# Optimization experiments

Measured on AMD Instinct MI355X. Metric: run time of the kernel, lower is better.

Reference implementation:

```python
import jax, jax.numpy as jnp
import numpy as np
import math

BT, N, D, H = 16, 1024, 128, 8
HD = D // H


def setup_inputs() -> dict:
    key = jax.random.key(0)
    ks = jax.random.split(key, 12)
    s = 1.0 / math.sqrt(D)
    return {
        "x": jax.random.normal(ks[0], (BT, N, D), dtype=jnp.float32),
        "adj": jax.random.uniform(ks[1], (BT, N, N), dtype=jnp.float32),
        "Wq": jax.random.normal(ks[2], (D, D), dtype=jnp.float32) * s,
        "bq": jax.random.normal(ks[3], (D,), dtype=jnp.float32) * 0.01,
        "Wk": jax.random.normal(ks[4], (D, D), dtype=jnp.float32) * s,
        "bk": jax.random.normal(ks[5], (D,), dtype=jnp.float32) * 0.01,
        "Wv": jax.random.normal(ks[6], (D, D), dtype=jnp.float32) * s,
        "bv": jax.random.normal(ks[7], (D,), dtype=jnp.float32) * 0.01,
        "Wo": jax.random.normal(ks[8], (D, D), dtype=jnp.float32) * s,
        "bo": jax.random.normal(ks[9], (D,), dtype=jnp.float32) * 0.01,
    }


def reference(x, adj, Wq, bq, Wk, bk, Wv, bv, Wo, bo):
    bt, n, d = x.shape
    # projections (torch Linear: x @ W.T + b), split into heads -> (BT,H,N,HD)
    q = (x @ Wq.T + bq).reshape(bt, n, H, HD).transpose(0, 2, 1, 3)
    k = (x @ Wk.T + bk).reshape(bt, n, H, HD).transpose(0, 2, 1, 3)
    v = (x @ Wv.T + bv).reshape(bt, n, H, HD).transpose(0, 2, 1, 3)
    scores = jnp.einsum('bhnd,bhmd->bhnm', q, k) / math.sqrt(HD)  # (BT,H,N,N)
    mask = (adj == 0)[:, None, :, :]  # (BT,1,N,N)
    scores = jnp.where(mask, -jnp.inf, scores)
    attn = jax.nn.softmax(scores, axis=-1)
    attn = attn * adj[:, None, :, :]  # reweight by continuous causal strength
    attn = attn / (attn.sum(axis=-1, keepdims=True) + 1e-8)  # renormalize
    ctx = jnp.einsum('bhnm,bhmd->bhnd', attn, v)  # (BT,H,N,HD)
    ctx = ctx.transpose(0, 2, 1, 3).reshape(bt, n, d)
    return ctx @ Wo.T + bo
```

## Files before the change

kernel.cpp:

```cpp
#include <hip/hip_runtime.h>
#include <hip/hip_bf16.h>

#define BTC 16
#define NC 1024
#define DC 128
#define HC 8
#define HDC 16

typedef __attribute__((ext_vector_type(8))) short bf16x8;
typedef __attribute__((ext_vector_type(4))) float f32x4;
typedef __attribute__((ext_vector_type(4))) short short4v;

#if __has_builtin(__builtin_amdgcn_exp2f)
#define EXP2F(x) __builtin_amdgcn_exp2f(x)
#else
#define EXP2F(x) exp2f(x)
#endif

#define QSCALE 0.36067376022224085f

union PK2 { short4v s4; __hip_bfloat162 h2[2]; };
union PK8 { bf16x8 v; short s[8]; __hip_bfloat162 h2[4]; };

static __device__ inline short f2bf(float f) {
    unsigned u = __builtin_bit_cast(unsigned, f);
    u += 0x7fffu + ((u >> 16) & 1u);
    return (short)(u >> 16);
}

static __device__ inline bf16x8 zero8() {
    PK8 f;
#pragma unroll
    for (int j = 0; j < 8; ++j) f.s[j] = 0;
    return f.v;
}

__global__ __launch_bounds__(256)
void prep_kernel(const float* __restrict__ x,
                 const float* __restrict__ Wq, const float* __restrict__ Wk,
                 const float* __restrict__ Wv, const float* __restrict__ Wo,
                 short* __restrict__ xbf, short* __restrict__ Wbf)
{
    int gid  = blockIdx.x * 256 + threadIdx.x;
    int base = gid * 4;
    const float* src;
    short* dst;
    if (base < 2097152) {
        src = x + base; dst = xbf + base;
    } else {
        int idx = base - 2097152;
        int w   = idx >> 14;
        int off = idx & 16383;
        src = ((w == 0) ? Wq : (w == 1) ? Wk : (w == 2) ? Wv : Wo) + off;
        dst = Wbf + w * 16384 + off;
    }
    float4 v = *(const float4*)src;
    PK2 pk;
    pk.h2[0] = __float22bfloat162_rn(make_float2(v.x, v.y));
    pk.h2[1] = __float22bfloat162_rn(make_float2(v.z, v.w));
    *(short4v*)dst = pk.s4;
}

__global__ __launch_bounds__(256)
void proj_qkv(const short* __restrict__ xbf, const short* __restrict__ Wbf,
              const float* __restrict__ bq, const float* __restrict__ bk,
              const float* __restrict__ bv,
              short* __restrict__ qo, short* __restrict__ ko, short* __restrict__ vto)
{
    const int y = blockIdx.y;
    const short* W = Wbf + y * 16384;
    const float* bias = (y == 0) ? bq : (y == 1) ? bk : bv;
    const float scale = (y == 0) ? QSCALE : 1.0f;

    const int tid  = threadIdx.x;
    const int wave = tid >> 6;
    const int lane = tid & 63;
    const int l15  = lane & 15;
    const int quad = lane >> 4;
    const int rowA = blockIdx.x * 64 + wave * 16;

    f32x4 acc[8];
#pragma unroll
    for (int t = 0; t < 8; ++t) acc[t] = (f32x4){0.f, 0.f, 0.f, 0.f};

#pragma unroll
    for (int kk = 0; kk < DC; kk += 32) {
        bf16x8 Af = *(const bf16x8*)&xbf[(size_t)(rowA + l15) * DC + kk + quad * 8];
#pragma unroll
        for (int t = 0; t < 8; ++t) {
            bf16x8 Bf = *(const bf16x8*)&W[(t * 16 + l15) * DC + kk + quad * 8];
            acc[t] = __builtin_amdgcn_mfma_f32_16x16x32_bf16(Af, Bf, acc[t], 0, 0, 0);
        }
    }

#pragma unroll
    for (int t = 0; t < 8; ++t) {
        int c = t * 16 + l15;
        float b = bias[c];
#pragma unroll
        for (int r = 0; r < 4; ++r) {
            int row = rowA + quad * 4 + r;
            float val = (acc[t][r] + b) * scale;
            if (y == 2)
                vto[(size_t)(row >> 10) * 131072 + (size_t)c * 1024 + (row & 1023)] = f2bf(val);
            else
                ((y == 0) ? qo : ko)[(size_t)row * DC + c] = f2bf(val);
        }
    }
}

__global__ __launch_bounds__(256)
void proj_out(const short* __restrict__ cbf, const short* __restrict__ Wobf,
              const float* __restrict__ bo, float* __restrict__ out)
{
    const int tid  = threadIdx.x;
    const int wave = tid >> 6;
    const int lane = tid & 63;
    const int l15  = lane & 15;
    const int quad = lane >> 4;
    const int rowA = blockIdx.x * 64 + wave * 16;

    f32x4 acc[8];
#pragma unroll
    for (int t = 0; t < 8; ++t) acc[t] = (f32x4){0.f, 0.f, 0.f, 0.f};

#pragma unroll
    for (int kk = 0; kk < DC; kk += 32) {
        bf16x8 Af = *(const bf16x8*)&cbf[(size_t)(rowA + l15) * DC + kk + quad * 8];
#pragma unroll
        for (int t = 0; t < 8; ++t) {
            bf16x8 Bf = *(const bf16x8*)&Wobf[(t * 16 + l15) * DC + kk + quad * 8];
            acc[t] = __builtin_amdgcn_mfma_f32_16x16x32_bf16(Af, Bf, acc[t], 0, 0, 0);
        }
    }

#pragma unroll
    for (int t = 0; t < 8; ++t) {
        int c = t * 16 + l15;
        float b = bo[c];
#pragma unroll
        for (int r = 0; r < 4; ++r) {
            int row = rowA + quad * 4 + r;
            out[(size_t)row * DC + c] = acc[t][r] + b;
        }
    }
}

__global__ __launch_bounds__(512)
void attn_kernel(const short* __restrict__ qb, const short* __restrict__ kb,
                 const short* __restrict__ vt, const float* __restrict__ adj,
                 short* __restrict__ cb)
{
    __shared__ float As[2][32 * 36];
    __shared__ short Ps[8 * 32 * 40];

    const int tid  = threadIdx.x;
    const int wave = tid >> 6;
    const int lane = tid & 63;
    const int l15  = lane & 15;
    const int quad = lane >> 4;
    const int bt   = blockIdx.y;
    const int qt0  = blockIdx.x * 32;
    const int h    = wave;

    const size_t xb = (size_t)bt * NC * DC;
    const size_t ab = (size_t)bt * NC * NC;

    bf16x8 Bq[2];
#pragma unroll
    for (int s = 0; s < 2; ++s)
        Bq[s] = (quad < 2)
            ? *(const bf16x8*)&qb[xb + (size_t)(qt0 + s * 16 + l15) * DC + h * HDC + quad * 8]
            : zero8();

    PK8 ones;
#pragma unroll
    for (int j = 0; j < 8; ++j) ones.s[j] = (short)0x3F80;

    f32x4 Cc[2], Cw[2];
#pragma unroll
    for (int s = 0; s < 2; ++s) {
        Cc[s] = (f32x4){0.f, 0.f, 0.f, 0.f};
        Cw[s] = (f32x4){0.f, 0.f, 0.f, 0.f};
    }

    const int arow = tid >> 4;
    const int acol = (tid & 15) * 2;
    const float* aptr = adj + ab + (size_t)(qt0 + arow) * NC + acol;
    float2 ar = *(const float2*)aptr;
    int p = 0;
    short* Pw = Ps + wave * 1280;

    for (int jt = 0; jt < NC; jt += 32) {
        *(float2*)&As[p][arow * 36 + acol] = ar;
        if (jt + 32 < NC) ar = *(const float2*)(aptr + jt + 32);
        __syncthreads();

        bf16x8 Ak[2];
#pragma unroll
        for (int g = 0; g < 2; ++g)
            Ak[g] = (quad < 2)
                ? *(const bf16x8*)&kb[xb + (size_t)(jt + g * 16 + l15) * DC + h * HDC + quad * 8]
                : zero8();
        bf16x8 Bv = *(const bf16x8*)&vt[((size_t)bt * DC + h * HDC + l15) * NC + jt + quad * 8];

        const f32x4 z4 = (f32x4){0.f, 0.f, 0.f, 0.f};
        f32x4 S[2][2];
#pragma unroll
        for (int s = 0; s < 2; ++s)
#pragma unroll
            for (int g = 0; g < 2; ++g)
                S[s][g] = __builtin_amdgcn_mfma_f32_16x16x32_bf16(Ak[g], Bq[s], z4, 0, 0, 0);

#pragma unroll
        for (int s = 0; s < 2; ++s)
#pragma unroll
            for (int g = 0; g < 2; ++g) {
                float4 a4 = *(const float4*)&As[p][(s * 16 + l15) * 36 + g * 16 + quad * 4];
                float p0 = EXP2F(S[s][g][0]) * a4.x;
                float p1 = EXP2F(S[s][g][1]) * a4.y;
                float p2 = EXP2F(S[s][g][2]) * a4.z;
                float p3 = EXP2F(S[s][g][3]) * a4.w;
                PK2 pk;
                pk.h2[0] = __float22bfloat162_rn(make_float2(p0, p1));
                pk.h2[1] = __float22bfloat162_rn(make_float2(p2, p3));
                *(short4v*)&Pw[(s * 16 + l15) * 40 + g * 16 + quad * 4] = pk.s4;
            }
        __builtin_amdgcn_wave_barrier();

#pragma unroll
        for (int s = 0; s < 2; ++s) {
            bf16x8 Ap = *(const bf16x8*)&Pw[(s * 16 + l15) * 40 + quad * 8];
            Cc[s] = __builtin_amdgcn_mfma_f32_16x16x32_bf16(Ap, Bv, Cc[s], 0, 0, 0);
            Cw[s] = __builtin_amdgcn_mfma_f32_16x16x32_bf16(Ap, ones.v, Cw[s], 0, 0, 0);
        }
        p ^= 1;
    }

#pragma unroll
    for (int s = 0; s < 2; ++s)
#pragma unroll
        for (int r = 0; r < 4; ++r) {
            float den = Cw[s][r];
            float rcp = den > 0.f ? 1.f / den : 0.f;
            int row = qt0 + s * 16 + quad * 4 + r;
            cb[xb + (size_t)row * DC + h * HDC + l15] = f2bf(Cc[s][r] * rcp);
        }
}

extern "C" void kernel_launch(void* const* d_in, const int* in_sizes, int n_in,
                              void* d_out, int out_size, void* d_ws, size_t ws_size,
                              hipStream_t stream)
{
    const float* x   = (const float*)d_in[0];
    const float* adj = (const float*)d_in[1];
    const float* Wq  = (const float*)d_in[2];
    const float* bq  = (const float*)d_in[3];
    const float* Wk  = (const float*)d_in[4];
    const float* bk  = (const float*)d_in[5];
    const float* Wv  = (const float*)d_in[6];
    const float* bv  = (const float*)d_in[7];
    const float* Wo  = (const float*)d_in[8];
    const float* bo  = (const float*)d_in[9];
    float* out = (float*)d_out;

    const size_t tok = (size_t)BTC * NC * DC;
    short* xbf  = (short*)d_ws;
    short* Wbf  = xbf  + tok;
    short* qbuf = Wbf  + 65536;
    short* kbuf = qbuf + tok;
    short* vt   = kbuf + tok;
    short* cbuf = vt   + tok;

    prep_kernel<<<2112, 256, 0, stream>>>(x, Wq, Wk, Wv, Wo, xbf, Wbf);

    dim3 pgrid(256, 3);
    proj_qkv<<<pgrid, 256, 0, stream>>>(xbf, Wbf, bq, bk, bv, qbuf, kbuf, vt);

    dim3 agrid(32, 16);
    attn_kernel<<<agrid, 512, 0, stream>>>(qbuf, kbuf, vt, adj, cbuf);

    proj_out<<<256, 256, 0, stream>>>(cbuf, Wbf + 3 * 16384, bo, out);
}
```

Before: 178.0 us.

## Use 32x32 MFMA for scores, register-prefetch adj/K/V, split heads across blocks

The attention kernel now computes the 32x32 score tile with a single 32x32x16 MFMA instead of four padded 16x16x32 ones, which removes the wasted half-zero operands. Adjacency values are loaded straight into registers and software-prefetched one tile ahead, dropping the shared-memory staging and block-wide __syncthreads. Heads are split over a third grid dimension so blocks have 256 threads with occupancy hints. Each head-block now reads adj from global memory itself, so adj traffic doubles and relies on cache. The V-transpose store in the projection also goes through shared memory to give coalesced vector writes.

Measured after the change: 221.1 us. 24.3% more time.

```diff
diff --git a/kernel.cpp b/kernel.cpp
--- a/kernel.cpp
+++ b/kernel.cpp
@@ -9,6 +9,7 @@
 
 typedef __attribute__((ext_vector_type(8))) short bf16x8;
 typedef __attribute__((ext_vector_type(4))) float f32x4;
+typedef __attribute__((ext_vector_type(16))) float f32x16;
 typedef __attribute__((ext_vector_type(4))) short short4v;
 
 #if __has_builtin(__builtin_amdgcn_exp2f)
@@ -26,13 +27,6 @@
     unsigned u = __builtin_bit_cast(unsigned, f);
     u += 0x7fffu + ((u >> 16) & 1u);
     return (short)(u >> 16);
-}
-
-static __device__ inline bf16x8 zero8() {
-    PK8 f;
-#pragma unroll
-    for (int j = 0; j < 8; ++j) f.s[j] = 0;
-    return f.v;
 }
 
 __global__ __launch_bounds__(256)
@@ -67,6 +61,8 @@
               const float* __restrict__ bv,
               short* __restrict__ qo, short* __restrict__ ko, short* __restrict__ vto)
 {
+    __shared__ short T[128 * 72];
+
     const int y = blockIdx.y;
     const short* W = Wbf + y * 16384;
     const float* bias = (y == 0) ? bq : (y == 1) ? bk : bv;
@@ -93,18 +89,38 @@
         }
     }
 
-#pragma unroll
-    for (int t = 0; t < 8; ++t) {
-        int c = t * 16 + l15;
-        float b = bias[c];
-#pragma unroll
-        for (int r = 0; r < 4; ++r) {
-            int row = rowA + quad * 4 + r;
-            float val = (acc[t][r] + b) * scale;
-            if (y == 2)
-                vto[(size_t)(row >> 10) * 131072 + (size_t)c * 1024 + (row & 1023)] = f2bf(val);
-            else
+    if (y == 2) {
+#pragma unroll
+        for (int t = 0; t < 8; ++t) {
+            int c = t * 16 + l15;
+            float b = bias[c];
+            PK2 pk;
+            pk.h2[0] = __float22bfloat162_rn(make_float2(acc[t][0] + b, acc[t][1] + b));
+            pk.h2[1] = __float22bfloat162_rn(make_float2(acc[t][2] + b, acc[t][3] + b));
+            *(short4v*)&T[c * 72 + wave * 16 + quad * 4] = pk.s4;
+        }
+        __syncthreads();
+        const int bt = blockIdx.x >> 4;
+        const int n0 = (blockIdx.x * 64) & 1023;
+        const int chunk = tid & 7;
+        const int dr    = tid >> 3;
+#pragma unroll
+        for (int rep = 0; rep < 4; ++rep) {
+            int d = rep * 32 + dr;
+            bf16x8 u = *(const bf16x8*)&T[d * 72 + chunk * 8];
+            *(bf16x8*)&vto[((size_t)bt * DC + d) * NC + n0 + chunk * 8] = u;
+        }
+    } else {
+#pragma unroll
+        for (int t = 0; t < 8; ++t) {
+            int c = t * 16 + l15;
+            float b = bias[c];
+#pragma unroll
+            for (int r = 0; r < 4; ++r) {
+                int row = rowA + quad * 4 + r;
+                float val = (acc[t][r] + b) * scale;
                 ((y == 0) ? qo : ko)[(size_t)row * DC + c] = f2bf(val);
+            }
         }
     }
 }
@@ -146,32 +162,28 @@
     }
 }
 
-__global__ __launch_bounds__(512)
+__global__ __launch_bounds__(256, 4)
 void attn_kernel(const short* __restrict__ qb, const short* __restrict__ kb,
                  const short* __restrict__ vt, const float* __restrict__ adj,
                  short* __restrict__ cb)
 {
-    __shared__ float As[2][32 * 36];
-    __shared__ short Ps[8 * 32 * 40];
+    __shared__ short Ps[4][32 * 40];
 
     const int tid  = threadIdx.x;
     const int wave = tid >> 6;
     const int lane = tid & 63;
+    const int l31  = lane & 31;
+    const int hi   = lane >> 5;
     const int l15  = lane & 15;
     const int quad = lane >> 4;
     const int bt   = blockIdx.y;
     const int qt0  = blockIdx.x * 32;
-    const int h    = wave;
+    const int h    = blockIdx.z * 4 + wave;
 
     const size_t xb = (size_t)bt * NC * DC;
     const size_t ab = (size_t)bt * NC * NC;
 
-    bf16x8 Bq[2];
-#pragma unroll
-    for (int s = 0; s < 2; ++s)
-        Bq[s] = (quad < 2)
-            ? *(const bf16x8*)&qb[xb + (size_t)(qt0 + s * 16 + l15) * DC + h * HDC + quad * 8]
-            : zero8();
+    const bf16x8 Bq = *(const bf16x8*)&qb[xb + (size_t)(qt0 + l31) * DC + h * HDC + hi * 8];
 
     PK8 ones;
 #pragma unroll
@@ -184,48 +196,49 @@
         Cw[s] = (f32x4){0.f, 0.f, 0.f, 0.f};
     }
 
-    const int arow = tid >> 4;
-    const int acol = (tid & 15) * 2;
-    const float* aptr = adj + ab + (size_t)(qt0 + arow) * NC + acol;
-    float2 ar = *(const float2*)aptr;
-    int p = 0;
-    short* Pw = Ps + wave * 1280;
+    short* Pw = &Ps[wave][0];
+
+    const short* kp = kb + xb + h * HDC + hi * 8;
+    const short* vp = vt + ((size_t)bt * DC + h * HDC + l15) * NC;
+    const float* ap = adj + ab + (size_t)(qt0 + l31) * NC + hi * 4;
+
+    bf16x8 Ak = *(const bf16x8*)&kp[(size_t)l31 * DC];
+    bf16x8 Bv = *(const bf16x8*)&vp[quad * 8];
+    float4 a0 = *(const float4*)&ap[0];
+    float4 a1 = *(const float4*)&ap[8];
+    float4 a2 = *(const float4*)&ap[16];
+    float4 a3 = *(const float4*)&ap[24];
 
     for (int jt = 0; jt < NC; jt += 32) {
-        *(float2*)&As[p][arow * 36 + acol] = ar;
-        if (jt + 32 < NC) ar = *(const float2*)(aptr + jt + 32);
-        __syncthreads();
-
-        bf16x8 Ak[2];
-#pragma unroll
-        for (int g = 0; g < 2; ++g)
-            Ak[g] = (quad < 2)
-                ? *(const bf16x8*)&kb[xb + (size_t)(jt + g * 16 + l15) * DC + h * HDC + quad * 8]
-                : zero8();
-        bf16x8 Bv = *(const bf16x8*)&vt[((size_t)bt * DC + h * HDC + l15) * NC + jt + quad * 8];
-
-        const f32x4 z4 = (f32x4){0.f, 0.f, 0.f, 0.f};
-        f32x4 S[2][2];
-#pragma unroll
-        for (int s = 0; s < 2; ++s)
-#pragma unroll
-            for (int g = 0; g < 2; ++g)
-                S[s][g] = __builtin_amdgcn_mfma_f32_16x16x32_bf16(Ak[g], Bq[s], z4, 0, 0, 0);
-
-#pragma unroll
-        for (int s = 0; s < 2; ++s)
-#pragma unroll
-            for (int g = 0; g < 2; ++g) {
-                float4 a4 = *(const float4*)&As[p][(s * 16 + l15) * 36 + g * 16 + quad * 4];
-                float p0 = EXP2F(S[s][g][0]) * a4.x;
-                float p1 = EXP2F(S[s][g][1]) * a4.y;
-                float p2 = EXP2F(S[s][g][2]) * a4.z;
-                float p3 = EXP2F(S[s][g][3]) * a4.w;
-                PK2 pk;
-                pk.h2[0] = __float22bfloat162_rn(make_float2(p0, p1));
-                pk.h2[1] = __float22bfloat162_rn(make_float2(p2, p3));
-                *(short4v*)&Pw[(s * 16 + l15) * 40 + g * 16 + quad * 4] = pk.s4;
-            }
+        const int nj = (jt + 32) & (NC - 1);
+        bf16x8 Akn = *(const bf16x8*)&kp[(size_t)(nj + l31) * DC];
+        bf16x8 Bvn = *(const bf16x8*)&vp[nj + quad * 8];
+        float4 b0  = *(const float4*)&ap[nj + 0];
+        float4 b1  = *(const float4*)&ap[nj + 8];
+        float4 b2  = *(const float4*)&ap[nj + 16];
+        float4 b3  = *(const float4*)&ap[nj + 24];
+
+        f32x16 S;
+#pragma unroll
+        for (int i = 0; i < 16; ++i) S[i] = 0.f;
+        S = __builtin_amdgcn_mfma_f32_32x32x16_bf16(Ak, Bq, S, 0, 0, 0);
+
+#define EXPGRP(t, A)                                                          \
+        {                                                                     \
+            float p0 = EXP2F(S[4*t+0]) * A.x;                                 \
+            float p1 = EXP2F(S[4*t+1]) * A.y;                                 \
+            float p2 = EXP2F(S[4*t+2]) * A.z;                                 \
+            float p3 = EXP2F(S[4*t+3]) * A.w;                                 \
+            PK2 pk;                                                           \
+            pk.h2[0] = __float22bfloat162_rn(make_float2(p0, p1));            \
+            pk.h2[1] = __float22bfloat162_rn(make_float2(p2, p3));            \
+            *(short4v*)&Pw[l31 * 40 + t * 8 + hi * 4] = pk.s4;                \
+        }
+        EXPGRP(0, a0)
+        EXPGRP(1, a1)
+        EXPGRP(2, a2)
+        EXPGRP(3, a3)
+#undef EXPGRP
         __builtin_amdgcn_wave_barrier();
 
 #pragma unroll
@@ -234,7 +247,8 @@
             Cc[s] = __builtin_amdgcn_mfma_f32_16x16x32_bf16(Ap, Bv, Cc[s], 0, 0, 0);
             Cw[s] = __builtin_amdgcn_mfma_f32_16x16x32_bf16(Ap, ones.v, Cw[s], 0, 0, 0);
         }
-        p ^= 1;
+
+        Ak = Akn; Bv = Bvn; a0 = b0; a1 = b1; a2 = b2; a3 = b3;
     }
 
 #pragma unroll
@@ -277,8 +291,8 @@
     dim3 pgrid(256, 3);
     proj_qkv<<<pgrid, 256, 0, stream>>>(xbf, Wbf, bq, bk, bv, qbuf, kbuf, vt);
 
-    dim3 agrid(32, 16);
-    attn_kernel<<<agrid, 512, 0, stream>>>(qbuf, kbuf, vt, adj, cbuf);
+    dim3 agrid(32, 16, 2);
+    attn_kernel<<<agrid, 256, 0, stream>>>(qbuf, kbuf, vt, adj, cbuf);
 
     proj_out<<<256, 256, 0, stream>>>(cbuf, Wbf + 3 * 16384, bo, out);
 }
```
